# Kernel tuning notes

Measured on AMD Instinct MI355X. Metric: run time of the kernel, lower is better.

Reference implementation:

```python
import jax, jax.numpy as jnp
import numpy as np

KERNEL = 7  # median blur window size (odd)


def setup_inputs() -> dict:
    key = jax.random.key(0)
    # NCHW image batch, values in [0,1) like normalized images
    img = jax.random.uniform(key, (8, 3, 512, 512), dtype=jnp.float32)
    return {"img": img}


def _median_blur(img, k):
    # Matches kornia.filters.median_blur: zero padding ('same'), then median
    # over the k*k window. k*k is odd so the exact middle of the sorted
    # window equals torch.median's lower median.
    pad = k // 2
    b, c, h, w = img.shape
    x = jnp.pad(img, ((0, 0), (0, 0), (pad, pad), (pad, pad)))  # zero pad
    # unfold: [B, C, k*k, H, W] — same materialization as kornia's conv2d
    # with binary one-hot kernels. Loop is over the fixed k*k = 49 taps.
    patches = jnp.stack(
        [x[:, :, i:i + h, j:j + w] for i in range(k) for j in range(k)],
        axis=2,
    )
    mid = (k * k) // 2
    return jnp.sort(patches, axis=2)[:, :, mid]  # [B, C, H, W]


def reference(img):
    return _median_blur(img, KERNEL)
```

## Files before the change

kernel.cpp:

```cpp
#include <hip/hip_runtime.h>
#include <utility>

#define IMG_H 512
#define IMG_W 512

typedef _Float16 h2 __attribute__((ext_vector_type(2)));

__device__ __forceinline__ h2 h2min(h2 a, h2 b) { return __builtin_elementwise_min(a, b); }
__device__ __forceinline__ h2 h2max(h2 a, h2 b) { return __builtin_elementwise_max(a, b); }

struct Op { int kind, a, b; };
constexpr int NSLOT = 320;
constexpr int MAXOPS = 4096;
struct Prog { Op ops[MAXOPS]; int n; bool ok; };

constexpr int pow2ceil(int x) { int p = 1; while (p < x) p += p; return p; }

struct Builder {
    Op ops[MAXOPS] = {};
    int n = 0;
    bool pad[NSLOT] = {};
    bool init[NSLOT] = {};
    bool ok = true;

    constexpr void emit(int k, int a, int b) {
        if (n < MAXOPS) ops[n++] = Op{k, a, b}; else ok = false;
    }
    constexpr void load(int s, int c) { emit(2, s, c); pad[s] = false; init[s] = true; }
    constexpr void mov(int d, int s) {
        if (!init[s]) ok = false;
        emit(1, d, s); pad[d] = pad[s]; init[d] = true;
    }
    constexpr void mkpad(int s) { pad[s] = true; init[s] = true; }
    constexpr void ce_(int a, int b) {
        if (!init[a] || !init[b]) { ok = false; return; }
        if (pad[a] && pad[b]) return;
        if (!pad[a] && pad[b]) return;
        if (pad[a] && !pad[b]) {
            emit(1, a, b); pad[a] = false; pad[b] = true; return;
        }
        emit(0, a, b);
    }
    constexpr void maxin(int a, int b) {
        if (!init[a] || !init[b] || pad[a] || pad[b]) ok = false;
        emit(5, a, b);
    }
    constexpr void minin(int a, int b) {
        if (!init[a] || !init[b] || pad[a] || pad[b]) ok = false;
        emit(4, a, b);
    }
    constexpr void sort_run(int base, int len) {
        for (int p = 1; p < len; p += p)
            for (int k = p; k > 0; k /= 2)
                for (int j = k % p; j + k < len; j += k + k)
                    for (int i = 0; i < k; ++i)
                        if (i + j + k < len)
                            if ((i + j) / (p + p) == (i + j + k) / (p + p))
                                ce_(base + i + j, base + i + j + k);
    }
    constexpr void merge_stage(int base, int P) {
        int nn = 2 * P, p = P;
        for (int k = p; k > 0; k /= 2)
            for (int j = k % p; j + k < nn; j += k + k)
                for (int i = 0; i < k; ++i) {
                    int a = i + j, b = i + j + k;
                    if (b < nn && a / (p + p) == b / (p + p)) ce_(base + a, base + b);
                }
    }
    constexpr void load_col(int base, int c) {
        for (int r = 0; r < 7; ++r) load(base + r, c * 7 + r);
        sort_run(base, 7);
    }
    constexpr void place(int dst, int src, int len, int P) {
        for (int i = 0; i < len; ++i) mov(dst + i, src + i);
        for (int i = len; i < P; ++i) mkpad(dst + i);
    }
    constexpr void merge_to(int dst, int s1, int l1, int s2, int l2) {
        int P = pow2ceil(l1 > l2 ? l1 : l2);
        place(dst, s1, l1, P);
        place(dst + P, s2, l2, P);
        merge_stage(dst, P);
    }
    constexpr void select_med49(int T, int A, int B, int o) {
        for (int t = 0; t < 7; ++t) {
            mov(T + t, A + 17 + t);
            maxin(B + 6 - t, T + t);
        }
        mov(T + 7, A + 24);
        minin(T, T + 1); minin(T + 2, T + 3);
        minin(T + 4, T + 5); minin(T + 6, T + 7);
        minin(T, T + 2); minin(T + 4, T + 6);
        minin(T, T + 4);
        if (!init[T] || pad[T]) ok = false;
        emit(3, o, T);
    }
};

constexpr Prog build() {
    Builder b{};
    constexpr int F34 = 80, F56 = 112, FC = 144, FP12 = 176, FP78 = 208;
    constexpr int C42 = 240;
    constexpr int T0 = 304, T1 = 312;

    for (int c = 0; c < 10; ++c) b.load_col(8 * c, c);

    b.merge_to(F34, 8 * 3, 7, 8 * 4, 7);
    b.merge_to(F56, 8 * 5, 7, 8 * 6, 7);
    b.merge_to(FC, F34, 14, F56, 14);

    b.merge_to(FP12, 8 * 1, 7, 8 * 2, 7);
    b.merge_to(C42, FC, 28, FP12, 14);
    b.select_med49(T0, C42, 8 * 0, 0);
    b.select_med49(T1, C42, 8 * 7, 1);

    b.merge_to(FP78, 8 * 7, 7, 8 * 8, 7);
    b.merge_to(C42, FC, 28, FP78, 14);
    b.select_med49(T0, C42, 8 * 2, 2);
    b.select_med49(T1, C42, 8 * 9, 3);

    Prog p{};
    bool needed[NSLOT] = {};
    int kindr[MAXOPS] = {};
    bool keep[MAXOPS] = {};
    for (int t = b.n - 1; t >= 0; --t) {
        Op o = b.ops[t];
        if (o.kind == 3) { keep[t] = true; kindr[t] = 3; needed[o.b] = true; }
        else if (o.kind == 0) {
            bool na = needed[o.a], nb = needed[o.b];
            if (na && nb)      { keep[t] = true; kindr[t] = 0; }
            else if (na)       { keep[t] = true; kindr[t] = 4; needed[o.b] = true; }
            else if (nb)       { keep[t] = true; kindr[t] = 5; needed[o.a] = true; }
        } else if (o.kind == 1) {
            if (needed[o.a]) { keep[t] = true; kindr[t] = 1; needed[o.a] = false; needed[o.b] = true; }
        } else if (o.kind == 2) {
            if (needed[o.a]) { keep[t] = true; kindr[t] = 2; needed[o.a] = false; }
        } else if (o.kind == 4) {
            if (needed[o.a]) { keep[t] = true; kindr[t] = 4; needed[o.b] = true; }
        } else if (o.kind == 5) {
            if (needed[o.b]) { keep[t] = true; kindr[t] = 5; needed[o.a] = true; }
        }
    }
    p.n = 0;
    for (int t = 0; t < b.n; ++t)
        if (keep[t]) { p.ops[p.n] = b.ops[t]; p.ops[p.n].kind = kindr[t]; ++p.n; }
    p.ok = b.ok;
    return p;
}

constexpr Prog PROG = build();
static_assert(PROG.ok && PROG.n > 0 && PROG.n < MAXOPS, "program build failed");

template <int I>
__device__ __forceinline__ void step(h2* v, const h2* cols, h2* med) {
    constexpr Op o = PROG.ops[I];
    if constexpr (o.kind == 0) {
        h2 lo = h2min(v[o.a], v[o.b]);
        h2 hi = h2max(v[o.a], v[o.b]);
        v[o.a] = lo; v[o.b] = hi;
    } else if constexpr (o.kind == 1) v[o.a] = v[o.b];
    else if constexpr (o.kind == 2) v[o.a] = cols[o.b];
    else if constexpr (o.kind == 3) med[o.a] = v[o.b];
    else if constexpr (o.kind == 4) v[o.a] = h2min(v[o.a], v[o.b]);
    else v[o.b] = h2max(v[o.a], v[o.b]);
}

template <size_t... Is>
__device__ __forceinline__ void run_all(h2* v, const h2* cols, h2* med,
                                        std::index_sequence<Is...>) {
    (step<(int)Is>(v, cols, med), ...);
}

__global__ __launch_bounds__(256) void median7x7_kernel(
        const float* __restrict__ img, float* __restrict__ out) {
    const int bc = blockIdx.z;
    const int tx = threadIdx.x;
    const int ty = threadIdx.y;
    const int x0 = (blockIdx.x * 64 + tx) * 4;
    const int y  = (blockIdx.y * 4 + ty) * 2;

    const float* base = img + (size_t)bc * (IMG_H * IMG_W);
    const bool okl = (x0 >= 4);
    const bool okr = (x0 <= 504);
    const int xl = okl ? (x0 - 4) : 0;
    const int xr = okr ? (x0 + 4) : 504;

    h2 colv[70];
    float prv[10];
#pragma unroll
    for (int r = 0; r < 8; ++r) {
        const int yy = y - 3 + r;
        float4 L, M, R;
        if ((unsigned)yy < IMG_H) {
            const float* rp = base + (size_t)yy * IMG_W;
            L = *(const float4*)(rp + xl);
            M = *(const float4*)(rp + x0);
            R = *(const float4*)(rp + xr);
        } else {
            L = make_float4(0.f, 0.f, 0.f, 0.f); M = L; R = L;
        }
        float cur[10];
        cur[0] = okl ? L.y : 0.f; cur[1] = okl ? L.z : 0.f; cur[2] = okl ? L.w : 0.f;
        cur[3] = M.x; cur[4] = M.y; cur[5] = M.z; cur[6] = M.w;
        cur[7] = okr ? R.x : 0.f; cur[8] = okr ? R.y : 0.f; cur[9] = okr ? R.z : 0.f;
        if (r > 0) {
#pragma unroll
            for (int c = 0; c < 10; ++c)
                colv[c * 7 + (r - 1)] = (h2)__builtin_amdgcn_cvt_pkrtz(prv[c], cur[c]);
        }
#pragma unroll
        for (int c = 0; c < 10; ++c) prv[c] = cur[c];
    }

    h2 v[NSLOT];
    h2 med[4];
    run_all(v, colv, med, std::make_index_sequence<(size_t)PROG.n>{});

    float* op = out + (size_t)bc * (IMG_H * IMG_W) + (size_t)y * IMG_W + x0;
    *(float4*)op = make_float4((float)med[0].x, (float)med[1].x,
                               (float)med[2].x, (float)med[3].x);
    *(float4*)(op + IMG_W) = make_float4((float)med[0].y, (float)med[1].y,
                                         (float)med[2].y, (float)med[3].y);
}

extern "C" void kernel_launch(void* const* d_in, const int* in_sizes, int n_in,
                              void* d_out, int out_size, void* d_ws, size_t ws_size,
                              hipStream_t stream) {
    const float* img = (const float*)d_in[0];
    float* out = (float*)d_out;
    dim3 grid(2, 64, 24);
    dim3 block(64, 4, 1);
    hipLaunchKernelGGL(median7x7_kernel, grid, block, 0, stream, img, out);
}
```

Before: 94.12 us.

## Compute eight output columns per thread, reusing sorted column merges

Each thread now produces 8x2 outputs instead of 4x2, and loads 14 columns rather than 10. The constexpr sorting-network program is extended so that merged, sorted column groups (e.g. a 28-element core and 14-element pairs) are shared across more output positions. Column loads are interleaved with the selects to limit how many values are live at once. This amortises the merge work and redundant halo loads over more outputs. In exchange it raises register pressure (more slots and columns) and halves the grid, which may lower occupancy.

```diff
diff --git a/kernel.cpp b/kernel.cpp
--- a/kernel.cpp
+++ b/kernel.cpp
@@ -10,7 +10,7 @@
 __device__ __forceinline__ h2 h2max(h2 a, h2 b) { return __builtin_elementwise_max(a, b); }
 
 struct Op { int kind, a, b; };
-constexpr int NSLOT = 320;
+constexpr int NSLOT = 352;
 constexpr int MAXOPS = 4096;
 struct Prog { Op ops[MAXOPS]; int n; bool ok; };
 
@@ -98,25 +98,41 @@
 
 constexpr Prog build() {
     Builder b{};
-    constexpr int F34 = 80, F56 = 112, FC = 144, FP12 = 176, FP78 = 208;
-    constexpr int C42 = 240;
-    constexpr int T0 = 304, T1 = 312;
-
-    for (int c = 0; c < 10; ++c) b.load_col(8 * c, c);
-
-    b.merge_to(F34, 8 * 3, 7, 8 * 4, 7);
-    b.merge_to(F56, 8 * 5, 7, 8 * 6, 7);
-    b.merge_to(FC, F34, 14, F56, 14);
-
-    b.merge_to(FP12, 8 * 1, 7, 8 * 2, 7);
-    b.merge_to(C42, FC, 28, FP12, 14);
+    constexpr int M12 = 112, M34 = 128, M56 = 144, M78 = 160, M910 = 176, M1112 = 192;
+    constexpr int C28A = 208, C28B = 240, C42 = 272, T0 = 336, T1 = 344;
+
+    for (int c = 1; c <= 8; ++c) b.load_col(8 * c, c);
+    b.merge_to(M34, 8 * 3, 7, 8 * 4, 7);
+    b.merge_to(M56, 8 * 5, 7, 8 * 6, 7);
+    b.merge_to(C28A, M34, 14, M56, 14);
+    b.merge_to(M12, 8 * 1, 7, 8 * 2, 7);
+    b.merge_to(M78, 8 * 7, 7, 8 * 8, 7);
+
+    b.merge_to(C42, C28A, 28, M12, 14);
+    b.load_col(8 * 0, 0);
     b.select_med49(T0, C42, 8 * 0, 0);
     b.select_med49(T1, C42, 8 * 7, 1);
 
-    b.merge_to(FP78, 8 * 7, 7, 8 * 8, 7);
-    b.merge_to(C42, FC, 28, FP78, 14);
+    b.merge_to(C42, C28A, 28, M78, 14);
+    b.load_col(8 * 9, 9);
     b.select_med49(T0, C42, 8 * 2, 2);
     b.select_med49(T1, C42, 8 * 9, 3);
+
+    b.load_col(8 * 10, 10);
+    b.merge_to(M910, 8 * 9, 7, 8 * 10, 7);
+    b.merge_to(C28B, M78, 14, M910, 14);
+
+    b.merge_to(C42, C28B, 28, M56, 14);
+    b.select_med49(T0, C42, 8 * 4, 4);
+    b.load_col(8 * 11, 11);
+    b.select_med49(T1, C42, 8 * 11, 5);
+
+    b.load_col(8 * 12, 12);
+    b.merge_to(M1112, 8 * 11, 7, 8 * 12, 7);
+    b.merge_to(C42, C28B, 28, M1112, 14);
+    b.select_med49(T0, C42, 8 * 6, 6);
+    b.load_col(8 * 13, 13);
+    b.select_med49(T1, C42, 8 * 13, 7);
 
     Prog p{};
     bool needed[NSLOT] = {};
@@ -175,51 +191,57 @@
     const int bc = blockIdx.z;
     const int tx = threadIdx.x;
     const int ty = threadIdx.y;
-    const int x0 = (blockIdx.x * 64 + tx) * 4;
+    const int x0 = (blockIdx.x * 64 + tx) * 8;
     const int y  = (blockIdx.y * 4 + ty) * 2;
 
     const float* base = img + (size_t)bc * (IMG_H * IMG_W);
     const bool okl = (x0 >= 4);
-    const bool okr = (x0 <= 504);
+    const bool okr = (x0 <= 496);
     const int xl = okl ? (x0 - 4) : 0;
-    const int xr = okr ? (x0 + 4) : 504;
-
-    h2 colv[70];
-    float prv[10];
+    const int xr = okr ? (x0 + 8) : 504;
+
+    h2 colv[98];
+    float prv[14];
 #pragma unroll
     for (int r = 0; r < 8; ++r) {
         const int yy = y - 3 + r;
-        float4 L, M, R;
+        float4 Q0, Q1, Q2, Q3;
         if ((unsigned)yy < IMG_H) {
             const float* rp = base + (size_t)yy * IMG_W;
-            L = *(const float4*)(rp + xl);
-            M = *(const float4*)(rp + x0);
-            R = *(const float4*)(rp + xr);
+            Q0 = *(const float4*)(rp + xl);
+            Q1 = *(const float4*)(rp + x0);
+            Q2 = *(const float4*)(rp + x0 + 4);
+            Q3 = *(const float4*)(rp + xr);
         } else {
-            L = make_float4(0.f, 0.f, 0.f, 0.f); M = L; R = L;
-        }
-        float cur[10];
-        cur[0] = okl ? L.y : 0.f; cur[1] = okl ? L.z : 0.f; cur[2] = okl ? L.w : 0.f;
-        cur[3] = M.x; cur[4] = M.y; cur[5] = M.z; cur[6] = M.w;
-        cur[7] = okr ? R.x : 0.f; cur[8] = okr ? R.y : 0.f; cur[9] = okr ? R.z : 0.f;
+            Q0 = make_float4(0.f, 0.f, 0.f, 0.f); Q1 = Q0; Q2 = Q0; Q3 = Q0;
+        }
+        float cur[14];
+        cur[0] = okl ? Q0.y : 0.f; cur[1] = okl ? Q0.z : 0.f; cur[2] = okl ? Q0.w : 0.f;
+        cur[3] = Q1.x; cur[4] = Q1.y; cur[5] = Q1.z; cur[6] = Q1.w;
+        cur[7] = Q2.x; cur[8] = Q2.y; cur[9] = Q2.z; cur[10] = Q2.w;
+        cur[11] = okr ? Q3.x : 0.f; cur[12] = okr ? Q3.y : 0.f; cur[13] = okr ? Q3.z : 0.f;
         if (r > 0) {
 #pragma unroll
-            for (int c = 0; c < 10; ++c)
+            for (int c = 0; c < 14; ++c)
                 colv[c * 7 + (r - 1)] = (h2)__builtin_amdgcn_cvt_pkrtz(prv[c], cur[c]);
         }
 #pragma unroll
-        for (int c = 0; c < 10; ++c) prv[c] = cur[c];
+        for (int c = 0; c < 14; ++c) prv[c] = cur[c];
     }
 
     h2 v[NSLOT];
-    h2 med[4];
+    h2 med[8];
     run_all(v, colv, med, std::make_index_sequence<(size_t)PROG.n>{});
 
     float* op = out + (size_t)bc * (IMG_H * IMG_W) + (size_t)y * IMG_W + x0;
     *(float4*)op = make_float4((float)med[0].x, (float)med[1].x,
                                (float)med[2].x, (float)med[3].x);
+    *(float4*)(op + 4) = make_float4((float)med[4].x, (float)med[5].x,
+                                     (float)med[6].x, (float)med[7].x);
     *(float4*)(op + IMG_W) = make_float4((float)med[0].y, (float)med[1].y,
                                          (float)med[2].y, (float)med[3].y);
+    *(float4*)(op + IMG_W + 4) = make_float4((float)med[4].y, (float)med[5].y,
+                                             (float)med[6].y, (float)med[7].y);
 }
 
 extern "C" void kernel_launch(void* const* d_in, const int* in_sizes, int n_in,
@@ -227,7 +249,7 @@
                               hipStream_t stream) {
     const float* img = (const float*)d_in[0];
     float* out = (float*)d_out;
-    dim3 grid(2, 64, 24);
+    dim3 grid(1, 64, 24);
     dim3 block(64, 4, 1);
     hipLaunchKernelGGL(median7x7_kernel, grid, block, 0, stream, img, out);
 }
```

Result: faster. 88.68 us (-5.8%).
